# Kernel optimization log

Measured on AMD Instinct MI355X. Metric: run time of the kernel, lower is better.

## Reference

```python
import jax, jax.numpy as jnp
import numpy as np

R = 40            # guided-filter radius (81x81 window)
EPS = 1e-3
BETA = 2.996 / 300.0  # visibility_m = 300.0


def _box_sum(x, r=R):
    """Zero-padded sliding-window sum over an (B,C,H,W) tensor.
    Matches F.avg_pool2d(x, 2r+1, stride=1, padding=r) * (2r+1)^2
    (count_include_pad=True), computed in O(HW) via prefix sums."""
    B, C, H, W = x.shape

    def _along(y, axis, L):
        cs = jnp.cumsum(y, axis=axis)
        pad = [(0, 0)] * 4
        pad[axis] = (1, 0)
        cs = jnp.pad(cs, pad)  # cs[i] = sum of first i elements
        hi = jnp.clip(jnp.arange(L) + r + 1, 0, L)
        lo = jnp.clip(jnp.arange(L) - r, 0, L)
        return jnp.take(cs, hi, axis=axis) - jnp.take(cs, lo, axis=axis)

    x = _along(x, 2, H)
    x = _along(x, 3, W)
    return x


def _guided_filter(I, p, r=R, eps=EPS):
    N = (2 * r + 1) ** 2
    mean_I = _box_sum(I, r) / N
    mean_p = _box_sum(p, r) / N
    mean_Ip = _box_sum(I * p, r) / N
    cov_Ip = mean_Ip - mean_I * mean_p
    mean_II = _box_sum(I * I, r) / N
    var_I = mean_II - mean_I * mean_I
    a = cov_Ip / (var_I + eps)
    b = mean_p - a * mean_I
    mean_a = _box_sum(a, r) / N
    mean_b = _box_sum(b, r) / N
    return mean_a * I + mean_b


def setup_inputs() -> dict:
    key = jax.random.key(0)
    k1, k2 = jax.random.split(key)
    B, H, W = 8, 768, 1280
    img = jax.random.uniform(k1, (B, 3, H, W), dtype=jnp.float32)
    depth = jax.random.uniform(k2, (B, 1, H, W), dtype=jnp.float32) * 500.0
    return {"img": img, "depth": depth}


def reference(img, depth):
    B, _, H, W = img.shape
    t_raw = jnp.clip(jnp.exp(-BETA * depth), 0.0, 1.0)          # (B,1,H,W)
    gray = (0.299 * img[:, 0:1] + 0.587 * img[:, 1:2]
            + 0.114 * img[:, 2:3])                               # (B,1,H,W)
    t = _guided_filter(gray, t_raw)                               # (B,1,H,W)

    # atmospheric light A: mean color over the k farthest pixels, per image
    k = max(10, int(0.001 * H * W))
    k = min(k, H * W)
    depth_flat = depth.reshape(B, -1)                             # (B,HW)
    img_flat = img.reshape(B, 3, -1)                              # (B,3,HW)
    _, idx = jax.lax.top_k(depth_flat, k)                         # (B,k)
    A = jnp.take_along_axis(img_flat, idx[:, None, :], axis=2).mean(axis=2)
    A = A.reshape(B, 3, 1, 1)

    return img * t + A * (1.0 - t)
```

## Files before the change

kernel.cpp:

```cpp
#include <hip/hip_runtime.h>
#include <hip/hip_fp16.h>
#include <stdint.h>

typedef unsigned int u32;

#define Bn 8
#define Hn 768
#define Wn 1280
#define HWs (Hn*Wn)
#define Rr 40
#define NNinv (1.0f/6561.0f)
#define KTOP 983
#define BETA_C (2.996f/300.0f)
#define EQCAP 4096
#define TK_BPI 480
#define NCH 96
#define SEGV 16
#define NSEGV 48
#define HIMG 4
#define TK1_WAVES 16
#define TW 640
#define CW 680

#define OFF_F     0
#define OFF_AB1   (16*HWs)
#define OFF_AB2   (24*HWs)
#define OFF_CS4f  (32*HWs)
#define OFF_CS2f  (36*HWs)
#define OFF_TAILf (38*HWs)

#define OFFH_FOVF 0
#define OFFH_AB   (4*HWs)
#define CS_N      (HIMG*NCH*Wn)
#define OFFH_CS4  (12*HWs)
#define OFFH_CS2  (OFFH_CS4 + 4*CS_N)
#define OFFH_TAIL (OFFH_CS2 + 2*CS_N)

#define ZERO_U32  (Bn*4096 + Bn*65536 + Bn)
#define ZERO_U4   (ZERO_U32/4 + 1)

__device__ __forceinline__ float4 f4add(float4 a, float4 b){ return make_float4(a.x+b.x,a.y+b.y,a.z+b.z,a.w+b.w); }
__device__ __forceinline__ float4 f4sub(float4 a, float4 b){ return make_float4(a.x-b.x,a.y-b.y,a.z-b.z,a.w-b.w); }

__device__ __forceinline__ u32 h2_to_u32(__half2 h){ union { __half2 h; u32 u; } c; c.h = h; return c.u; }
__device__ __forceinline__ __half2 u32_to_h2(u32 u){ union { u32 u; __half2 h; } c; c.u = u; return c.h; }

__global__ __launch_bounds__(256) void fill0_kernel(uint4* __restrict__ p){
  int i = blockIdx.x*256 + threadIdx.x;
  if (i < ZERO_U4) p[i] = make_uint4(0,0,0,0);
}


__global__ __launch_bounds__(256) void gA_kernel(const float* __restrict__ img, const float* __restrict__ depth,
    uint2* __restrict__ F, float4* __restrict__ CS4){
  __shared__ float4 lds[769];
  __shared__ float4 wtot[4];
  int blk = blockIdx.x;
  int xt = blk & 1;
  int t2 = blk >> 1;
  int b = t2 / NCH, ch = t2 % NCH;
  int x0 = xt*TW;
  int cstart = xt ? (TW - Rr) : 0;
  int tid = threadIdx.x;
  int lane = tid & 63, wv = tid >> 6;
  float4 acc[3];
  #pragma unroll
  for (int j = 0; j < 3; ++j) acc[j] = make_float4(0,0,0,0);

  const float* irB = img + ((size_t)(b*3+0)*Hn + ch*8)*Wn + cstart;
  const float* igB = img + ((size_t)(b*3+1)*Hn + ch*8)*Wn + cstart;
  const float* ibB = img + ((size_t)(b*3+2)*Hn + ch*8)*Wn + cstart;
  const float* dpB = depth + ((size_t)b*Hn + ch*8)*Wn + cstart;

  float pr[3], pg[3], pb[3], pd[3];
  #pragma unroll
  for (int j = 0; j < 3; ++j){
    int i = tid + j*256;
    if (i < CW){ pr[j]=irB[i]; pg[j]=igB[i]; pb[j]=ibB[i]; pd[j]=dpB[i]; }
  }

  for (int r = 0; r < 8; ++r){
    int y = ch*8 + r;
    __syncthreads();
    #pragma unroll
    for (int j = 0; j < 3; ++j){
      int i = tid + j*256;
      float4 f = make_float4(0,0,0,0);
      if (i < CW){
        float I = 0.299f*pr[j] + 0.587f*pg[j] + 0.114f*pb[j];
        float p = fminf(fmaxf(expf(-BETA_C*pd[j]), 0.0f), 1.0f);
        f = make_float4(I, p, I*p, I*I);
      }
      lds[i] = f;
    }
    if (r < 7){
      size_t off = (size_t)(r+1)*Wn;
      #pragma unroll
      for (int j = 0; j < 3; ++j){
        int i = tid + j*256;
        if (i < CW){ pr[j]=irB[off+i]; pg[j]=igB[off+i]; pb[j]=ibB[off+i]; pd[j]=dpB[off+i]; }
      }
    }
    __syncthreads();
    int base = tid*3;
    float4 loc[3]; float4 tsum = make_float4(0,0,0,0);
    #pragma unroll
    for (int j = 0; j < 3; ++j){ loc[j] = lds[base+j]; tsum = f4add(tsum, loc[j]); }
    float4 v = tsum;
    for (int d = 1; d < 64; d <<= 1){
      float4 o; o.x = __shfl_up(v.x, d); o.y = __shfl_up(v.y, d); o.z = __shfl_up(v.z, d); o.w = __shfl_up(v.w, d);
      if (lane >= d) v = f4add(v, o);
    }
    if (lane == 63) wtot[wv] = v;
    __syncthreads();
    float4 ex = f4sub(v, tsum);
    for (int w = 0; w < wv; ++w) ex = f4add(ex, wtot[w]);
    float4 run = ex;
    #pragma unroll
    for (int j = 0; j < 3; ++j){ lds[base+j] = run; run = f4add(run, loc[j]); }
    __syncthreads();
    #pragma unroll
    for (int j = 0; j < 3; ++j){
      int lx = tid + j*256;
      if (lx < TW){
        int gx = x0 + lx;
        int hi = gx + Rr + 1; if (hi > Wn) hi = Wn;
        int lo = gx - Rr;     if (lo < 0)  lo = 0;
        float4 s = f4sub(lds[hi - cstart], lds[lo - cstart]);
        __half2 h01 = __float22half2_rn(make_float2(s.x, s.y));
        __half2 h23 = __float22half2_rn(make_float2(s.z, s.w));
        F[(size_t)b*HWs + (size_t)y*Wn + gx] = make_uint2(h2_to_u32(h01), h2_to_u32(h23));
        float2 f0 = __half22float2(h01), f1 = __half22float2(h23);
        acc[j] = f4add(acc[j], make_float4(f0.x, f0.y, f1.x, f1.y));
      }
    }
  }
  #pragma unroll
  for (int j = 0; j < 3; ++j){
    int lx = tid + j*256;
    if (lx < TW) CS4[((size_t)b*NCH + ch)*Wn + x0 + lx] = acc[j];
  }
}

__global__ __launch_bounds__(256) void vAf_kernel(const uint2* __restrict__ F, const float4* __restrict__ CS,
    u32* __restrict__ AB){
  int gt = blockIdx.x*256 + threadIdx.x;
  int x  = gt % Wn;
  int t2 = gt / Wn;
  int b = t2 % Bn, s = t2 / Bn;
  const uint2* Fb   = F + (size_t)b*HWs;
  const float4* CSb = CS + (size_t)b*NCH*Wn;
  int y0 = s*SEGV;
  int c0 = 2*s - 5; if (c0 < 0) c0 = 0;
  int c1 = 2*s + 5; if (c1 > NCH) c1 = NCH;
  float4 S = make_float4(0,0,0,0);
  for (int c = c0; c < c1; ++c) S = f4add(S, CSb[(size_t)c*Wn + x]);
  u32* ABb = AB + (size_t)b*HWs;
  #pragma unroll 8
  for (int y = y0; y < y0 + SEGV; ++y){
    int ya = y + Rr;
    if (ya < Hn){
      uint2 u = Fb[(size_t)ya*Wn + x];
      float2 f0 = __half22float2(u32_to_h2(u.x)), f1 = __half22float2(u32_to_h2(u.y));
      S.x += f0.x; S.y += f0.y; S.z += f1.x; S.w += f1.y;
    }
    float mI = S.x*NNinv, mp = S.y*NNinv, mIp = S.z*NNinv, mII = S.w*NNinv;
    float var = mII - mI*mI;
    float a  = (mIp - mI*mp) / (var + 1e-3f);
    float bb = mp - a*mI;
    ABb[(size_t)y*Wn + x] = h2_to_u32(__float22half2_rn(make_float2(a, bb)));
    int yb = y - Rr;
    if (yb >= 0){
      uint2 u = Fb[(size_t)yb*Wn + x];
      float2 f0 = __half22float2(u32_to_h2(u.x)), f1 = __half22float2(u32_to_h2(u.y));
      S.x -= f0.x; S.y -= f0.y; S.z -= f1.x; S.w -= f1.y;
    }
  }
}

__global__ __launch_bounds__(256) void gB_kernel(const u32* __restrict__ AB1, u32* __restrict__ AB2,
    float2* __restrict__ CS2){
  __shared__ float2 lds[769];
  __shared__ float2 wtot[4];
  int blk = blockIdx.x;
  int xt = blk & 1;
  int t2 = blk >> 1;
  int b = t2 / NCH, ch = t2 % NCH;
  int x0 = xt*TW;
  int cstart = xt ? (TW - Rr) : 0;
  int tid = threadIdx.x;
  int lane = tid & 63, wv = tid >> 6;
  float2 acc[3];
  #pragma unroll
  for (int j = 0; j < 3; ++j) acc[j] = make_float2(0,0);

  const u32* rowB = AB1 + (size_t)b*HWs + (size_t)(ch*8)*Wn + cstart;
  u32 pv[3];
  #pragma unroll
  for (int j = 0; j < 3; ++j){
    int i = tid + j*256;
    if (i < CW) pv[j] = rowB[i];
  }

  for (int r = 0; r < 8; ++r){
    int y = ch*8 + r;
    __syncthreads();
    #pragma unroll
    for (int j = 0; j < 3; ++j){
      int i = tid + j*256;
      float2 f = make_float2(0,0);
      if (i < CW) f = __half22float2(u32_to_h2(pv[j]));
      lds[i] = f;
    }
    if (r < 7){
      size_t off = (size_t)(r+1)*Wn;
      #pragma unroll
      for (int j = 0; j < 3; ++j){
        int i = tid + j*256;
        if (i < CW) pv[j] = rowB[off+i];
      }
    }
    __syncthreads();
    int base = tid*3;
    float2 loc[3]; float2 tsum = make_float2(0,0);
    #pragma unroll
    for (int j = 0; j < 3; ++j){ loc[j] = lds[base+j]; tsum.x += loc[j].x; tsum.y += loc[j].y; }
    float2 v = tsum;
    for (int d = 1; d < 64; d <<= 1){
      float2 o; o.x = __shfl_up(v.x, d); o.y = __shfl_up(v.y, d);
      if (lane >= d){ v.x += o.x; v.y += o.y; }
    }
    if (lane == 63) wtot[wv] = v;
    __syncthreads();
    float2 ex = make_float2(v.x - tsum.x, v.y - tsum.y);
    for (int w = 0; w < wv; ++w){ ex.x += wtot[w].x; ex.y += wtot[w].y; }
    float2 run = ex;
    #pragma unroll
    for (int j = 0; j < 3; ++j){ lds[base+j] = run; run.x += loc[j].x; run.y += loc[j].y; }
    __syncthreads();
    #pragma unroll
    for (int j = 0; j < 3; ++j){
      int lx = tid + j*256;
      if (lx < TW){
        int gx = x0 + lx;
        int hi = gx + Rr + 1; if (hi > Wn) hi = Wn;
        int lo = gx - Rr;     if (lo < 0)  lo = 0;
        float2 s = make_float2(lds[hi - cstart].x - lds[lo - cstart].x,
                               lds[hi - cstart].y - lds[lo - cstart].y);
        __half2 h = __float22half2_rn(s);
        AB2[(size_t)b*HWs + (size_t)y*Wn + gx] = h2_to_u32(h);
        float2 fr = __half22float2(h);
        acc[j].x += fr.x; acc[j].y += fr.y;
      }
    }
  }
  #pragma unroll
  for (int j = 0; j < 3; ++j){
    int lx = tid + j*256;
    if (lx < TW) CS2[((size_t)b*NCH + ch)*Wn + x0 + lx] = acc[j];
  }
}

__global__ __launch_bounds__(256) void vBf_kernel(const u32* __restrict__ AB2, const float2* __restrict__ CS,
    const float* __restrict__ img, const float* __restrict__ Avec, float* __restrict__ out){
  int gt = blockIdx.x*256 + threadIdx.x;
  int x  = gt % Wn;
  int t2 = gt / Wn;
  int b = t2 % Bn, s = t2 / Bn;
  const u32* ABb = AB2 + (size_t)b*HWs;
  const float2* CSb = CS + (size_t)b*NCH*Wn;
  int y0 = s*SEGV;
  int c0 = 2*s - 5; if (c0 < 0) c0 = 0;
  int c1 = 2*s + 5; if (c1 > NCH) c1 = NCH;
  float2 S = make_float2(0,0);
// ... 10 lines not shown
    int ya = y + Rr;
    if (ya < Hn){ float2 t = __half22float2(u32_to_h2(ABb[(size_t)ya*Wn + x])); S.x += t.x; S.y += t.y; }
    float ma = S.x*NNinv, mb = S.y*NNinv;
    size_t idx = (size_t)y*Wn + x;
    float r = ir[idx], g = ig[idx], bb = ib[idx];
    float gray = 0.299f*r + 0.587f*g + 0.114f*bb;
    float t = ma*gray + mb;
    o0[idx] = r *t + A0*(1.0f - t);
    o1[idx] = g *t + A1*(1.0f - t);
    o2[idx] = bb*t + A2*(1.0f - t);
    int yb = y - Rr;
    if (yb >= 0){ float2 t2v = __half22float2(u32_to_h2(ABb[(size_t)yb*Wn + x])); S.x -= t2v.x; S.y -= t2v.y; }
  }
}


__global__ __launch_bounds__(256) void hA_kernel(const float* __restrict__ img, const float* __restrict__ depth,
    float4* __restrict__ Fd, float4* __restrict__ Fw, int half){
  __shared__ float4 lds[Wn+1];
  __shared__ float4 wtot[4];
  int blk = blockIdx.x;
  int bl = blk / Hn, y = blk % Hn;
  int b = half*HIMG + bl;
  const float* ir = img + ((size_t)(b*3+0)*Hn + y)*Wn;
  const float* ig = img + ((size_t)(b*3+1)*Hn + y)*Wn;
  const float* ib = img + ((size_t)(b*3+2)*Hn + y)*Wn;
  const float* dp = depth + ((size_t)b*Hn + y)*Wn;
  int tid = threadIdx.x;
  for (int i = tid; i < Wn; i += 256){
    float r = ir[i], g = ig[i], bb = ib[i];
// ... 142 lines not shown
    if (ya < Hn){ float2 t = ABb[(size_t)ya*Wn + x]; S.x += t.x; S.y += t.y; }
    float ma = S.x*NNinv, mb = S.y*NNinv;
    size_t idx = (size_t)y*Wn + x;
    float r = ir[idx], g = ig[idx], bb = ib[idx];
    float gray = 0.299f*r + 0.587f*g + 0.114f*bb;
    float t = ma*gray + mb;
    o0[idx] = r *t + A0*(1.0f - t);
    o1[idx] = g *t + A1*(1.0f - t);
    o2[idx] = bb*t + A2*(1.0f - t);
    int yb = y - Rr;
    if (yb >= 0){ float2 t2v = ABb[(size_t)yb*Wn + x]; S.x -= t2v.x; S.y -= t2v.y; }
  }
}


__global__ __launch_bounds__(1024) void tk1_kernel(const float* __restrict__ depth, u32* __restrict__ hist1){
  __shared__ u32 lh[TK1_WAVES*2048];
  int tid = threadIdx.x;
  for (int i = tid; i < TK1_WAVES*2048; i += 1024) lh[i] = 0;
  __syncthreads();
  int b = blockIdx.x >> 5;
  int slice = blockIdx.x & 31;
  const int per = HWs/32;
  int start = b*HWs + slice*per;
  u32* h = &lh[(tid >> 6) * 2048];
  const float2* dp = (const float2*)(depth + start);
  for (int i = tid; i < per/2; i += 1024){
    float2 v = dp[i];
    u32 u0 = __float_as_uint(v.x), u1 = __float_as_uint(v.y);
    u32 b0 = u0 >> 20, b1 = u1 >> 20;
    atomicAdd(&h[b0 >> 1], (b0 & 1u) ? 65536u : 1u);
    atomicAdd(&h[b1 >> 1], (b1 & 1u) ? 65536u : 1u);
  }
  __syncthreads();
  for (int i = tid; i < 4096; i += 1024){
    u32 s = 0;
    for (int w = 0; w < TK1_WAVES; ++w) s += (lh[w*2048 + (i>>1)] >> ((i&1)*16)) & 0xFFFFu;
    if (s) atomicAdd(&hist1[b*4096+i], s);
  }
}

__global__ __launch_bounds__(256) void tk2_kernel(const u32* __restrict__ hist1,
    u32* __restrict__ selP1, u32* __restrict__ selK1){
  int b = blockIdx.x, tid = threadIdx.x;
  const u32* h = hist1 + b*4096;
  u32 cs = 0; int bb = tid*16;
  for (int i = 0; i < 16; ++i) cs += h[bb+i];
  __shared__ u32 sums[256];
  sums[tid] = cs; __syncthreads();
  u32 above = 0;
  for (int t = tid+1; t < 256; ++t) above += sums[t];
  if (above < KTOP && above + cs >= KTOP){
    u32 acc = above;
    for (int i = 15; i >= 0; --i){
      u32 c = h[bb+i]; acc += c;
      if (acc >= KTOP){ selP1[b] = (u32)(bb+i); selK1[b] = KTOP - (acc - c); break; }
    }
  }
}

__global__ __launch_bounds__(256) void tk3_kernel(const float* __restrict__ depth,
    const u32* __restrict__ selP1, u32* __restrict__ hist2){
  int idx = blockIdx.x*2048 + threadIdx.x;
  int b = blockIdx.x / TK_BPI;
  u32 p1 = selP1[b];
  for (int it = 0; it < 8; ++it, idx += 256){
    u32 u = __float_as_uint(depth[idx]);
    if ((u>>20) == p1) atomicAdd(&hist2[b*65536 + ((u>>4)&0xFFFFu)], 1u);
  }
}

__global__ __launch_bounds__(256) void tk4_kernel(const u32* __restrict__ hist2, const u32* __restrict__ selP1,
    const u32* __restrict__ selK1, u32* __restrict__ selTau, u32* __restrict__ selK2){
  int b = blockIdx.x, tid = threadIdx.x;
  const u32* h = hist2 + b*65536;
  u32 kk = selK1[b];
  u32 cs = 0; int bb = tid*256;
  for (int i = 0; i < 256; ++i) cs += h[bb+i];
  __shared__ u32 sums[256];
  sums[tid] = cs; __syncthreads();
  u32 above = 0;
  for (int t = tid+1; t < 256; ++t) above += sums[t];
  if (above < kk && above + cs >= kk){
    u32 acc = above;
    for (int i = 255; i >= 0; --i){
      u32 c = h[bb+i]; acc += c;
      if (acc >= kk){ selTau[b] = (selP1[b]<<16) | (u32)(bb+i); selK2[b] = kk - (acc - c); break; }
    }
  }
}

__global__ __launch_bounds__(256) void tk5_kernel(const float* __restrict__ depth, const float* __restrict__ img,
    const u32* __restrict__ selTau, u32* __restrict__ eqCount, u32* __restrict__ eqVal, u32* __restrict__ eqIdx,
    float* __restrict__ partial){
  int blk = blockIdx.x;
  int b = blk / TK_BPI;
  u32 tau = selTau[b];
  int idx = blk*2048 + threadIdx.x;
  float cr = 0.f, cg = 0.f, cb = 0.f;
  for (int it = 0; it < 8; ++it, idx += 256){
    int pix = idx - b*HWs;
    u32 u = __float_as_uint(depth[idx]);
    u32 u28 = u >> 4;
    if (u28 > tau){
      cr += img[(size_t)(b*3+0)*HWs + pix];
      cg += img[(size_t)(b*3+1)*HWs + pix];
      cb += img[(size_t)(b*3+2)*HWs + pix];
    } else if (u28 == tau){
      u32 p = atomicAdd(&eqCount[b], 1u);
      if (p < EQCAP){ eqVal[b*EQCAP+p] = u; eqIdx[b*EQCAP+p] = (u32)pix; }
    }
  }
  for (int d = 32; d; d >>= 1){
    cr += __shfl_down(cr, d); cg += __shfl_down(cg, d); cb += __shfl_down(cb, d);
  }
  __shared__ float wsum[4][3];
  int lane = threadIdx.x & 63, wv = threadIdx.x >> 6;
  if (lane == 0){ wsum[wv][0] = cr; wsum[wv][1] = cg; wsum[wv][2] = cb; }
  __syncthreads();
  if (threadIdx.x == 0){
    float r = 0.f, g = 0.f, bl = 0.f;
    for (int w = 0; w < 4; ++w){ r += wsum[w][0]; g += wsum[w][1]; bl += wsum[w][2]; }
    partial[blk*3+0] = r; partial[blk*3+1] = g; partial[blk*3+2] = bl;
  }
}

__global__ void tk6_kernel(const float* __restrict__ img, const u32* __restrict__ eqCount,
    u32* __restrict__ eqVal, const u32* __restrict__ eqIdx, const u32* __restrict__ selK2,
    const float* __restrict__ partial, float* __restrict__ Avec){
  int b = blockIdx.x;
  int tid = threadIdx.x;
  float r = 0.f, g = 0.f, bl = 0.f;
  for (int i = tid; i < TK_BPI; i += 64){
    r  += partial[(b*TK_BPI+i)*3+0];
    g  += partial[(b*TK_BPI+i)*3+1];
    bl += partial[(b*TK_BPI+i)*3+2];
  }
  for (int d = 32; d; d >>= 1){
    r += __shfl_down(r, d); g += __shfl_down(g, d); bl += __shfl_down(bl, d);
  }
  if (tid != 0) return;
  u32 m = eqCount[b]; if (m > EQCAP) m = EQCAP;
  u32 need = selK2[b]; if (need > m) need = m;
  float cr = r, cg = g, cb = bl;
  for (u32 it = 0; it < need; ++it){
    int best = -1; u32 bv = 0, bi = 0;
    for (u32 j = 0; j < m; ++j){
      u32 vv = eqVal[b*EQCAP+j];
      if (vv == 0xFFFFFFFFu) continue;
      u32 ix = eqIdx[b*EQCAP+j];
      if (best < 0 || vv > bv || (vv == bv && ix < bi)){ best = (int)j; bv = vv; bi = ix; }
    }
    eqVal[b*EQCAP+best] = 0xFFFFFFFFu;
    cr += img[(size_t)(b*3+0)*HWs + bi];
    cg += img[(size_t)(b*3+1)*HWs + bi];
    cb += img[(size_t)(b*3+2)*HWs + bi];
  }
  float inv = 1.0f/(float)KTOP;
  Avec[b*3+0] = cr*inv; Avec[b*3+1] = cg*inv; Avec[b*3+2] = cb*inv;
}


extern "C" void kernel_launch(void* const* d_in, const int* in_sizes, int n_in,
                              void* d_out, int out_size, void* d_ws, size_t ws_size,
                              hipStream_t stream){
  const float* img   = (const float*)d_in[0];
  const float* depth = (const float*)d_in[1];
  float* out = (float*)d_out;
  float* ws  = (float*)d_ws;

  const size_t tailFloats = (size_t)ZERO_U32 + 4*Bn + 2*(size_t)Bn*EQCAP
                          + (size_t)Bn*TK_BPI*3 + Bn*3 + 16;
  const size_t needFull = ((size_t)38*HWs + tailFloats) * sizeof(float);
  bool full = (ws_size >= needFull);

  size_t offTail = full ? (size_t)OFF_TAILf : (size_t)OFFH_TAIL;
  u32* tail    = (u32*)(ws + offTail);
  u32* hist1   = tail;
  u32* hist2   = hist1 + Bn*4096;
  u32* eqCount = hist2 + (size_t)Bn*65536;
  u32* selP1   = eqCount + Bn;
  u32* selK1   = selP1 + Bn;
  u32* selTau  = selK1 + Bn;
  u32* selK2   = selTau + Bn;
  u32* eqVal   = selK2 + Bn;
  u32* eqIdx   = eqVal + (size_t)Bn*EQCAP;
  float* partial = (float*)(eqIdx + (size_t)Bn*EQCAP);
  float* Avec    = partial + (size_t)Bn*TK_BPI*3;

  fill0_kernel<<<dim3((ZERO_U4 + 255)/256), dim3(256), 0, stream>>>((uint4*)tail);

  tk1_kernel<<<dim3(Bn*32), dim3(1024), 0, stream>>>(depth, hist1);
  tk2_kernel<<<dim3(Bn),    dim3(256), 0, stream>>>(hist1, selP1, selK1);
  tk3_kernel<<<dim3(Bn*TK_BPI), dim3(256), 0, stream>>>(depth, selP1, hist2);
  tk4_kernel<<<dim3(Bn),    dim3(256), 0, stream>>>(hist2, selP1, selK1, selTau, selK2);
  tk5_kernel<<<dim3(Bn*TK_BPI), dim3(256), 0, stream>>>(depth, img, selTau, eqCount, eqVal, eqIdx, partial);
  tk6_kernel<<<dim3(Bn),    dim3(64),  0, stream>>>(img, eqCount, eqVal, eqIdx, selK2, partial, Avec);

  if (full){
    uint2*  F   = (uint2*)(ws + OFF_F);
    u32*    AB1 = (u32*)(ws + OFF_AB1);
    u32*    AB2 = (u32*)(ws + OFF_AB2);
    float4* CS4 = (float4*)(ws + OFF_CS4f);
    float2* CS2 = (float2*)(ws + OFF_CS2f);
    gA_kernel <<<dim3(Bn*NCH*2),            dim3(256), 0, stream>>>(img, depth, F, CS4);
    vAf_kernel<<<dim3((Bn*Wn*NSEGV)/256),   dim3(256), 0, stream>>>(F, CS4, AB1);
    gB_kernel <<<dim3(Bn*NCH*2),            dim3(256), 0, stream>>>(AB1, AB2, CS2);
    vBf_kernel<<<dim3((Bn*Wn*NSEGV)/256),   dim3(256), 0, stream>>>(AB2, CS2, img, Avec, out);
  } else {
    float4* Fw  = (float4*)(ws + OFFH_FOVF);
    float2* AB  = (float2*)(ws + OFFH_AB);
    float4* CS4 = (float4*)(ws + OFFH_CS4);
    float2* CS2 = (float2*)(ws + OFFH_CS2);
    for (int half = 0; half < 2; ++half){
      float4* Fd = (float4*)out + (size_t)half*3*HWs;
      hA_kernel <<<dim3(HIMG*Hn),            dim3(256), 0, stream>>>(img, depth, Fd, Fw, half);
      cs4_kernel<<<dim3((HIMG*NCH*Wn)/256),  dim3(256), 0, stream>>>(Fd, Fw, CS4);
      vA_kernel <<<dim3((HIMG*Wn*NSEGV)/256),dim3(256), 0, stream>>>(Fd, Fw, CS4, AB);
      hB_kernel <<<dim3(HIMG*Hn),            dim3(256), 0, stream>>>(AB);
      cs2_kernel<<<dim3((HIMG*NCH*Wn)/256),  dim3(256), 0, stream>>>(AB, CS2);
      vB_kernel <<<dim3((HIMG*Wn*NSEGV)/256),dim3(256), 0, stream>>>(AB, CS2, img, Avec, out, half);
    }
  }
}
// ... 1 lines not shown
```

Before: 220.4 us.

## Fuse top-k histogram passes into guided-filter kernels as extra blocks

Top-k selection stages tk1, tk3 and tk5 are merged into the guided-filter kernels gA, vAf and gB as extra blocks selected by blockIdx. Their independent work can then fill the GPU alongside the filter passes, and the separate launches disappear. The tk1 histogram now uses 256-thread blocks with 4 per-wave histograms instead of 16, and LDS is shared through a union. The fallback path keeps the original separate kernels, and extra LDS per block in gA may reduce occupancy.

```diff
diff --git a/kernel.cpp b/kernel.cpp
--- a/kernel.cpp
+++ b/kernel.cpp
@@ -18,9 +18,10 @@
 #define SEGV 16
 #define NSEGV 48
 #define HIMG 4
-#define TK1_WAVES 16
 #define TW 640
 #define CW 680
+#define NGA (Bn*NCH*2)
+#define NVF ((Bn*Wn*NSEGV)/256)
 
 #define OFF_F     0
 #define OFF_AB1   (16*HWs)
@@ -51,213 +52,282 @@
 }
 
 
-__global__ __launch_bounds__(256) void gA_kernel(const float* __restrict__ img, const float* __restrict__ depth,
-    uint2* __restrict__ F, float4* __restrict__ CS4){
-  __shared__ float4 lds[769];
-  __shared__ float4 wtot[4];
-  int blk = blockIdx.x;
-  int xt = blk & 1;
-  int t2 = blk >> 1;
-  int b = t2 / NCH, ch = t2 % NCH;
-  int x0 = xt*TW;
-  int cstart = xt ? (TW - Rr) : 0;
+__global__ __launch_bounds__(256) void gA_tk1_kernel(const float* __restrict__ img, const float* __restrict__ depth,
+    uint2* __restrict__ F, float4* __restrict__ CS4, u32* __restrict__ hist1){
+  __shared__ union SM {
+    u32 lh[8192];
+    struct { float4 lds[769]; float4 wtot[4]; } g;
+  } sm;
   int tid = threadIdx.x;
-  int lane = tid & 63, wv = tid >> 6;
-  float4 acc[3];
-  #pragma unroll
-  for (int j = 0; j < 3; ++j) acc[j] = make_float4(0,0,0,0);
-
-  const float* irB = img + ((size_t)(b*3+0)*Hn + ch*8)*Wn + cstart;
-  const float* igB = img + ((size_t)(b*3+1)*Hn + ch*8)*Wn + cstart;
-  const float* ibB = img + ((size_t)(b*3+2)*Hn + ch*8)*Wn + cstart;
-  const float* dpB = depth + ((size_t)b*Hn + ch*8)*Wn + cstart;
-
-  float pr[3], pg[3], pb[3], pd[3];
-  #pragma unroll
-  for (int j = 0; j < 3; ++j){
-    int i = tid + j*256;
-    if (i < CW){ pr[j]=irB[i]; pg[j]=igB[i]; pb[j]=ibB[i]; pd[j]=dpB[i]; }
-  }
-
-  for (int r = 0; r < 8; ++r){
-    int y = ch*8 + r;
-    __syncthreads();
+  if ((int)blockIdx.x < NGA){
+    int blk = blockIdx.x;
+    int xt = blk & 1;
+    int t2 = blk >> 1;
+    int b = t2 / NCH, ch = t2 % NCH;
+    int x0 = xt*TW;
+    int cstart = xt ? (TW - Rr) : 0;
+    int lane = tid & 63, wv = tid >> 6;
+    float4 acc[3];
+    #pragma unroll
+    for (int j = 0; j < 3; ++j) acc[j] = make_float4(0,0,0,0);
+    const float* irB = img + ((size_t)(b*3+0)*Hn + ch*8)*Wn + cstart;
+    const float* igB = img + ((size_t)(b*3+1)*Hn + ch*8)*Wn + cstart;
+    const float* ibB = img + ((size_t)(b*3+2)*Hn + ch*8)*Wn + cstart;
+    const float* dpB = depth + ((size_t)b*Hn + ch*8)*Wn + cstart;
+    float pr[3], pg[3], pb[3], pd[3];
     #pragma unroll
     for (int j = 0; j < 3; ++j){
       int i = tid + j*256;
-      float4 f = make_float4(0,0,0,0);
-      if (i < CW){
-        float I = 0.299f*pr[j] + 0.587f*pg[j] + 0.114f*pb[j];
-        float p = fminf(fmaxf(expf(-BETA_C*pd[j]), 0.0f), 1.0f);
-        f = make_float4(I, p, I*p, I*I);
-      }
-      lds[i] = f;
-    }
-    if (r < 7){
-      size_t off = (size_t)(r+1)*Wn;
+      if (i < CW){ pr[j]=irB[i]; pg[j]=igB[i]; pb[j]=ibB[i]; pd[j]=dpB[i]; }
+    }
+    for (int r = 0; r < 8; ++r){
+      int y = ch*8 + r;
+      __syncthreads();
       #pragma unroll
       for (int j = 0; j < 3; ++j){
         int i = tid + j*256;
-        if (i < CW){ pr[j]=irB[off+i]; pg[j]=igB[off+i]; pb[j]=ibB[off+i]; pd[j]=dpB[off+i]; }
-      }
-    }
-    __syncthreads();
-    int base = tid*3;
-    float4 loc[3]; float4 tsum = make_float4(0,0,0,0);
-    #pragma unroll
-    for (int j = 0; j < 3; ++j){ loc[j] = lds[base+j]; tsum = f4add(tsum, loc[j]); }
-    float4 v = tsum;
-    for (int d = 1; d < 64; d <<= 1){
-      float4 o; o.x = __shfl_up(v.x, d); o.y = __shfl_up(v.y, d); o.z = __shfl_up(v.z, d); o.w = __shfl_up(v.w, d);
-      if (lane >= d) v = f4add(v, o);
-    }
-    if (lane == 63) wtot[wv] = v;
-    __syncthreads();
-    float4 ex = f4sub(v, tsum);
-    for (int w = 0; w < wv; ++w) ex = f4add(ex, wtot[w]);
-    float4 run = ex;
-    #pragma unroll
-    for (int j = 0; j < 3; ++j){ lds[base+j] = run; run = f4add(run, loc[j]); }
-    __syncthreads();
+        float4 f = make_float4(0,0,0,0);
+        if (i < CW){
+          float I = 0.299f*pr[j] + 0.587f*pg[j] + 0.114f*pb[j];
+          float p = fminf(fmaxf(expf(-BETA_C*pd[j]), 0.0f), 1.0f);
+          f = make_float4(I, p, I*p, I*I);
+        }
+        sm.g.lds[i] = f;
+      }
+      if (r < 7){
+        size_t off = (size_t)(r+1)*Wn;
+        #pragma unroll
+        for (int j = 0; j < 3; ++j){
+          int i = tid + j*256;
+          if (i < CW){ pr[j]=irB[off+i]; pg[j]=igB[off+i]; pb[j]=ibB[off+i]; pd[j]=dpB[off+i]; }
+        }
+      }
+      __syncthreads();
+      int base = tid*3;
+      float4 loc[3]; float4 tsum = make_float4(0,0,0,0);
+      #pragma unroll
+      for (int j = 0; j < 3; ++j){ loc[j] = sm.g.lds[base+j]; tsum = f4add(tsum, loc[j]); }
+      float4 v = tsum;
+      for (int d = 1; d < 64; d <<= 1){
+        float4 o; o.x = __shfl_up(v.x, d); o.y = __shfl_up(v.y, d); o.z = __shfl_up(v.z, d); o.w = __shfl_up(v.w, d);
+        if (lane >= d) v = f4add(v, o);
+      }
+      if (lane == 63) sm.g.wtot[wv] = v;
+      __syncthreads();
+      float4 ex = f4sub(v, tsum);
+      for (int w = 0; w < wv; ++w) ex = f4add(ex, sm.g.wtot[w]);
+      float4 run = ex;
+      #pragma unroll
+      for (int j = 0; j < 3; ++j){ sm.g.lds[base+j] = run; run = f4add(run, loc[j]); }
+      __syncthreads();
+      #pragma unroll
+      for (int j = 0; j < 3; ++j){
+        int lx = tid + j*256;
+        if (lx < TW){
+          int gx = x0 + lx;
+          int hi = gx + Rr + 1; if (hi > Wn) hi = Wn;
+          int lo = gx - Rr;     if (lo < 0)  lo = 0;
+          float4 s = f4sub(sm.g.lds[hi - cstart], sm.g.lds[lo - cstart]);
+          __half2 h01 = __float22half2_rn(make_float2(s.x, s.y));
+          __half2 h23 = __float22half2_rn(make_float2(s.z, s.w));
+          F[(size_t)b*HWs + (size_t)y*Wn + gx] = make_uint2(h2_to_u32(h01), h2_to_u32(h23));
+          float2 f0 = __half22float2(h01), f1 = __half22float2(h23);
+          acc[j] = f4add(acc[j], make_float4(f0.x, f0.y, f1.x, f1.y));
+        }
+      }
+    }
     #pragma unroll
     for (int j = 0; j < 3; ++j){
       int lx = tid + j*256;
-      if (lx < TW){
-        int gx = x0 + lx;
-        int hi = gx + Rr + 1; if (hi > Wn) hi = Wn;
-        int lo = gx - Rr;     if (lo < 0)  lo = 0;
-        float4 s = f4sub(lds[hi - cstart], lds[lo - cstart]);
-        __half2 h01 = __float22half2_rn(make_float2(s.x, s.y));
-        __half2 h23 = __float22half2_rn(make_float2(s.z, s.w));
-        F[(size_t)b*HWs + (size_t)y*Wn + gx] = make_uint2(h2_to_u32(h01), h2_to_u32(h23));
-        float2 f0 = __half22float2(h01), f1 = __half22float2(h23);
-        acc[j] = f4add(acc[j], make_float4(f0.x, f0.y, f1.x, f1.y));
-      }
-    }
-  }
-  #pragma unroll
-  for (int j = 0; j < 3; ++j){
-    int lx = tid + j*256;
-    if (lx < TW) CS4[((size_t)b*NCH + ch)*Wn + x0 + lx] = acc[j];
-  }
-}
-
-__global__ __launch_bounds__(256) void vAf_kernel(const uint2* __restrict__ F, const float4* __restrict__ CS,
-    u32* __restrict__ AB){
-  int gt = blockIdx.x*256 + threadIdx.x;
-  int x  = gt % Wn;
-  int t2 = gt / Wn;
-  int b = t2 % Bn, s = t2 / Bn;
-  const uint2* Fb   = F + (size_t)b*HWs;
-  const float4* CSb = CS + (size_t)b*NCH*Wn;
-  int y0 = s*SEGV;
-  int c0 = 2*s - 5; if (c0 < 0) c0 = 0;
-  int c1 = 2*s + 5; if (c1 > NCH) c1 = NCH;
-  float4 S = make_float4(0,0,0,0);
-  for (int c = c0; c < c1; ++c) S = f4add(S, CSb[(size_t)c*Wn + x]);
-  u32* ABb = AB + (size_t)b*HWs;
-  #pragma unroll 8
-  for (int y = y0; y < y0 + SEGV; ++y){
-    int ya = y + Rr;
-    if (ya < Hn){
-      uint2 u = Fb[(size_t)ya*Wn + x];
-      float2 f0 = __half22float2(u32_to_h2(u.x)), f1 = __half22float2(u32_to_h2(u.y));
-      S.x += f0.x; S.y += f0.y; S.z += f1.x; S.w += f1.y;
-    }
-    float mI = S.x*NNinv, mp = S.y*NNinv, mIp = S.z*NNinv, mII = S.w*NNinv;
-    float var = mII - mI*mI;
-    float a  = (mIp - mI*mp) / (var + 1e-3f);
-    float bb = mp - a*mI;
-    ABb[(size_t)y*Wn + x] = h2_to_u32(__float22half2_rn(make_float2(a, bb)));
-    int yb = y - Rr;
-    if (yb >= 0){
-      uint2 u = Fb[(size_t)yb*Wn + x];
-      float2 f0 = __half22float2(u32_to_h2(u.x)), f1 = __half22float2(u32_to_h2(u.y));
-      S.x -= f0.x; S.y -= f0.y; S.z -= f1.x; S.w -= f1.y;
-    }
-  }
-}
-
-__global__ __launch_bounds__(256) void gB_kernel(const u32* __restrict__ AB1, u32* __restrict__ AB2,
-    float2* __restrict__ CS2){
-  __shared__ float2 lds[769];
-  __shared__ float2 wtot[4];
-  int blk = blockIdx.x;
-  int xt = blk & 1;
-  int t2 = blk >> 1;
-  int b = t2 / NCH, ch = t2 % NCH;
-  int x0 = xt*TW;
-  int cstart = xt ? (TW - Rr) : 0;
+      if (lx < TW) CS4[((size_t)b*NCH + ch)*Wn + x0 + lx] = acc[j];
+    }
+  } else {
+    for (int i = tid; i < 8192; i += 256) sm.lh[i] = 0;
+    __syncthreads();
+    int blk = blockIdx.x - NGA;
+    int b = blk >> 5;
+    int slice = blk & 31;
+    const int per = HWs/32;
+    int start = b*HWs + slice*per;
+    u32* h = &sm.lh[(tid >> 6) * 2048];
+    const float2* dp = (const float2*)(depth + start);
+    for (int i = tid; i < per/2; i += 256){
+      float2 v = dp[i];
+      u32 u0 = __float_as_uint(v.x), u1 = __float_as_uint(v.y);
+      u32 b0 = u0 >> 20, b1 = u1 >> 20;
+      atomicAdd(&h[b0 >> 1], (b0 & 1u) ? 65536u : 1u);
+      atomicAdd(&h[b1 >> 1], (b1 & 1u) ? 65536u : 1u);
+    }
+    __syncthreads();
+    for (int i = tid; i < 4096; i += 256){
+      u32 s = 0;
+      for (int w = 0; w < 4; ++w) s += (sm.lh[w*2048 + (i>>1)] >> ((i&1)*16)) & 0xFFFFu;
+      if (s) atomicAdd(&hist1[b*4096+i], s);
+    }
+  }
+}
+
+__global__ __launch_bounds__(256) void vAf_tk3_kernel(const uint2* __restrict__ F, const float4* __restrict__ CS,
+    u32* __restrict__ AB, const float* __restrict__ depth, const u32* __restrict__ selP1, u32* __restrict__ hist2){
+  if ((int)blockIdx.x < NVF){
+    int gt = blockIdx.x*256 + threadIdx.x;
+    int x  = gt % Wn;
+    int t2 = gt / Wn;
+    int b = t2 % Bn, s = t2 / Bn;
+    const uint2* Fb   = F + (size_t)b*HWs;
+    const float4* CSb = CS + (size_t)b*NCH*Wn;
+    int y0 = s*SEGV;
+    int c0 = 2*s - 5; if (c0 < 0) c0 = 0;
+    int c1 = 2*s + 5; if (c1 > NCH) c1 = NCH;
+    float4 S = make_float4(0,0,0,0);
+    for (int c = c0; c < c1; ++c) S = f4add(S, CSb[(size_t)c*Wn + x]);
+    u32* ABb = AB + (size_t)b*HWs;
+    #pragma unroll 8
+    for (int y = y0; y < y0 + SEGV; ++y){
+      int ya = y + Rr;
+      if (ya < Hn){
+        uint2 u = Fb[(size_t)ya*Wn + x];
+        float2 f0 = __half22float2(u32_to_h2(u.x)), f1 = __half22float2(u32_to_h2(u.y));
+        S.x += f0.x; S.y += f0.y; S.z += f1.x; S.w += f1.y;
+      }
+      float mI = S.x*NNinv, mp = S.y*NNinv, mIp = S.z*NNinv, mII = S.w*NNinv;
+      float var = mII - mI*mI;
+      float a  = (mIp - mI*mp) / (var + 1e-3f);
+      float bb = mp - a*mI;
+      ABb[(size_t)y*Wn + x] = h2_to_u32(__float22half2_rn(make_float2(a, bb)));
+      int yb = y - Rr;
+      if (yb >= 0){
+        uint2 u = Fb[(size_t)yb*Wn + x];
+        float2 f0 = __half22float2(u32_to_h2(u.x)), f1 = __half22float2(u32_to_h2(u.y));
+        S.x -= f0.x; S.y -= f0.y; S.z -= f1.x; S.w -= f1.y;
+      }
+    }
+  } else {
+    int blk = blockIdx.x - NVF;
+    int idx = blk*2048 + threadIdx.x;
+    int b = blk / TK_BPI;
+    u32 p1 = selP1[b];
+    for (int it = 0; it < 8; ++it, idx += 256){
+      u32 u = __float_as_uint(depth[idx]);
+      if ((u>>20) == p1) atomicAdd(&hist2[b*65536 + ((u>>4)&0xFFFFu)], 1u);
+    }
+  }
+}
+
+__global__ __launch_bounds__(256) void gB_tk5_kernel(const u32* __restrict__ AB1, u32* __restrict__ AB2,
+    float2* __restrict__ CS2, const float* __restrict__ depth, const float* __restrict__ img,
+    const u32* __restrict__ selTau, u32* __restrict__ eqCount, u32* __restrict__ eqVal, u32* __restrict__ eqIdx,
+    float* __restrict__ partial){
+  __shared__ union SM {
+    struct { float2 lds[769]; float2 wtot[4]; } g;
+    float wsum[12];
+  } sm;
   int tid = threadIdx.x;
-  int lane = tid & 63, wv = tid >> 6;
-  float2 acc[3];
-  #pragma unroll
-  for (int j = 0; j < 3; ++j) acc[j] = make_float2(0,0);
-
-  const u32* rowB = AB1 + (size_t)b*HWs + (size_t)(ch*8)*Wn + cstart;
-  u32 pv[3];
-  #pragma unroll
-  for (int j = 0; j < 3; ++j){
-    int i = tid + j*256;
-    if (i < CW) pv[j] = rowB[i];
-  }
-
-  for (int r = 0; r < 8; ++r){
-    int y = ch*8 + r;
-    __syncthreads();
+  if ((int)blockIdx.x < NGA){
+    int blk = blockIdx.x;
+    int xt = blk & 1;
+    int t2 = blk >> 1;
+    int b = t2 / NCH, ch = t2 % NCH;
+    int x0 = xt*TW;
+    int cstart = xt ? (TW - Rr) : 0;
+    int lane = tid & 63, wv = tid >> 6;
+    float2 acc[3];
+    #pragma unroll
+    for (int j = 0; j < 3; ++j) acc[j] = make_float2(0,0);
+    const u32* rowB = AB1 + (size_t)b*HWs + (size_t)(ch*8)*Wn + cstart;
+    u32 pv[3];
     #pragma unroll
     for (int j = 0; j < 3; ++j){
       int i = tid + j*256;
-      float2 f = make_float2(0,0);
-      if (i < CW) f = __half22float2(u32_to_h2(pv[j]));
-      lds[i] = f;
-    }
-    if (r < 7){
-      size_t off = (size_t)(r+1)*Wn;
+      if (i < CW) pv[j] = rowB[i];
+    }
+    for (int r = 0; r < 8; ++r){
+      int y = ch*8 + r;
+      __syncthreads();
       #pragma unroll
       for (int j = 0; j < 3; ++j){
         int i = tid + j*256;
-        if (i < CW) pv[j] = rowB[off+i];
-      }
-    }
-    __syncthreads();
-    int base = tid*3;
-    float2 loc[3]; float2 tsum = make_float2(0,0);
-    #pragma unroll
-    for (int j = 0; j < 3; ++j){ loc[j] = lds[base+j]; tsum.x += loc[j].x; tsum.y += loc[j].y; }
-    float2 v = tsum;
-    for (int d = 1; d < 64; d <<= 1){
-      float2 o; o.x = __shfl_up(v.x, d); o.y = __shfl_up(v.y, d);
-      if (lane >= d){ v.x += o.x; v.y += o.y; }
-    }
-    if (lane == 63) wtot[wv] = v;
-    __syncthreads();
-    float2 ex = make_float2(v.x - tsum.x, v.y - tsum.y);
-    for (int w = 0; w < wv; ++w){ ex.x += wtot[w].x; ex.y += wtot[w].y; }
-    float2 run = ex;
-    #pragma unroll
-    for (int j = 0; j < 3; ++j){ lds[base+j] = run; run.x += loc[j].x; run.y += loc[j].y; }
-    __syncthreads();
+        float2 f = make_float2(0,0);
+        if (i < CW) f = __half22float2(u32_to_h2(pv[j]));
+        sm.g.lds[i] = f;
+      }
+      if (r < 7){
+        size_t off = (size_t)(r+1)*Wn;
+        #pragma unroll
+        for (int j = 0; j < 3; ++j){
+          int i = tid + j*256;
+          if (i < CW) pv[j] = rowB[off+i];
+        }
+      }
+      __syncthreads();
+      int base = tid*3;
+      float2 loc[3]; float2 tsum = make_float2(0,0);
+      #pragma unroll
+      for (int j = 0; j < 3; ++j){ loc[j] = sm.g.lds[base+j]; tsum.x += loc[j].x; tsum.y += loc[j].y; }
+      float2 v = tsum;
+      for (int d = 1; d < 64; d <<= 1){
+        float2 o; o.x = __shfl_up(v.x, d); o.y = __shfl_up(v.y, d);
+        if (lane >= d){ v.x += o.x; v.y += o.y; }
+      }
+      if (lane == 63) sm.g.wtot[wv] = v;
+      __syncthreads();
+      float2 ex = make_float2(v.x - tsum.x, v.y - tsum.y);
+      for (int w = 0; w < wv; ++w){ ex.x += sm.g.wtot[w].x; ex.y += sm.g.wtot[w].y; }
+      float2 run = ex;
+      #pragma unroll
+      for (int j = 0; j < 3; ++j){ sm.g.lds[base+j] = run; run.x += loc[j].x; run.y += loc[j].y; }
+      __syncthreads();
+      #pragma unroll
+      for (int j = 0; j < 3; ++j){
+        int lx = tid + j*256;
+        if (lx < TW){
+          int gx = x0 + lx;
+          int hi = gx + Rr + 1; if (hi > Wn) hi = Wn;
+          int lo = gx - Rr;     if (lo < 0)  lo = 0;
+          float2 s = make_float2(sm.g.lds[hi - cstart].x - sm.g.lds[lo - cstart].x,
+                                 sm.g.lds[hi - cstart].y - sm.g.lds[lo - cstart].y);
+          __half2 h = __float22half2_rn(s);
+          AB2[(size_t)b*HWs + (size_t)y*Wn + gx] = h2_to_u32(h);
+          float2 fr = __half22float2(h);
+          acc[j].x += fr.x; acc[j].y += fr.y;
+        }
+      }
+    }
     #pragma unroll
     for (int j = 0; j < 3; ++j){
       int lx = tid + j*256;
-      if (lx < TW){
-        int gx = x0 + lx;
-        int hi = gx + Rr + 1; if (hi > Wn) hi = Wn;
-        int lo = gx - Rr;     if (lo < 0)  lo = 0;
-        float2 s = make_float2(lds[hi - cstart].x - lds[lo - cstart].x,
-                               lds[hi - cstart].y - lds[lo - cstart].y);
-        __half2 h = __float22half2_rn(s);
-        AB2[(size_t)b*HWs + (size_t)y*Wn + gx] = h2_to_u32(h);
-        float2 fr = __half22float2(h);
-        acc[j].x += fr.x; acc[j].y += fr.y;
-      }
-    }
-  }
-  #pragma unroll
-  for (int j = 0; j < 3; ++j){
-    int lx = tid + j*256;
-    if (lx < TW) CS2[((size_t)b*NCH + ch)*Wn + x0 + lx] = acc[j];
+      if (lx < TW) CS2[((size_t)b*NCH + ch)*Wn + x0 + lx] = acc[j];
+    }
+  } else {
+    int blk = blockIdx.x - NGA;
+    int b = blk / TK_BPI;
+    u32 tau = selTau[b];
+    int idx = blk*2048 + tid;
+    float cr = 0.f, cg = 0.f, cb = 0.f;
+    for (int it = 0; it < 8; ++it, idx += 256){
+      int pix = idx - b*HWs;
+      u32 u = __float_as_uint(depth[idx]);
+      u32 u28 = u >> 4;
+      if (u28 > tau){
+        cr += img[(size_t)(b*3+0)*HWs + pix];
+        cg += img[(size_t)(b*3+1)*HWs + pix];
+        cb += img[(size_t)(b*3+2)*HWs + pix];
+      } else if (u28 == tau){
+        u32 p = atomicAdd(&eqCount[b], 1u);
+        if (p < EQCAP){ eqVal[b*EQCAP+p] = u; eqIdx[b*EQCAP+p] = (u32)pix; }
+      }
+    }
+    for (int d = 32; d; d >>= 1){
+      cr += __shfl_down(cr, d); cg += __shfl_down(cg, d); cb += __shfl_down(cb, d);
+    }
+    int lane = tid & 63, wv = tid >> 6;
+    if (lane == 0){ sm.wsum[wv*3+0] = cr; sm.wsum[wv*3+1] = cg; sm.wsum[wv*3+2] = cb; }
+    __syncthreads();
+    if (tid == 0){
+      float r = 0.f, g = 0.f, bl = 0.f;
+      for (int w = 0; w < 4; ++w){ r += sm.wsum[w*3+0]; g += sm.wsum[w*3+1]; bl += sm.wsum[w*3+2]; }
+      partial[blk*3+0] = r; partial[blk*3+1] = g; partial[blk*3+2] = bl;
+    }
   }
 }
 
@@ -298,6 +368,153 @@
   }
 }
 
+
+__global__ __launch_bounds__(256) void tk2_kernel(const u32* __restrict__ hist1,
+    u32* __restrict__ selP1, u32* __restrict__ selK1){
+  int b = blockIdx.x, tid = threadIdx.x;
+  const u32* h = hist1 + b*4096;
+  u32 cs = 0; int bb = tid*16;
+  for (int i = 0; i < 16; ++i) cs += h[bb+i];
+  __shared__ u32 sums[256];
+  sums[tid] = cs; __syncthreads();
+  u32 above = 0;
+  for (int t = tid+1; t < 256; ++t) above += sums[t];
+  if (above < KTOP && above + cs >= KTOP){
+    u32 acc = above;
+    for (int i = 15; i >= 0; --i){
+      u32 c = h[bb+i]; acc += c;
+      if (acc >= KTOP){ selP1[b] = (u32)(bb+i); selK1[b] = KTOP - (acc - c); break; }
+    }
+  }
+}
+
+__global__ __launch_bounds__(256) void tk4_kernel(const u32* __restrict__ hist2, const u32* __restrict__ selP1,
+    const u32* __restrict__ selK1, u32* __restrict__ selTau, u32* __restrict__ selK2){
+  int b = blockIdx.x, tid = threadIdx.x;
+  const u32* h = hist2 + b*65536;
+  u32 kk = selK1[b];
+  u32 cs = 0; int bb = tid*256;
+  for (int i = 0; i < 256; ++i) cs += h[bb+i];
+  __shared__ u32 sums[256];
+  sums[tid] = cs; __syncthreads();
+  u32 above = 0;
+  for (int t = tid+1; t < 256; ++t) above += sums[t];
+  if (above < kk && above + cs >= kk){
+    u32 acc = above;
+    for (int i = 255; i >= 0; --i){
+      u32 c = h[bb+i]; acc += c;
+      if (acc >= kk){ selTau[b] = (selP1[b]<<16) | (u32)(bb+i); selK2[b] = kk - (acc - c); break; }
+    }
+  }
+}
+
+__global__ void tk6_kernel(const float* __restrict__ img, const u32* __restrict__ eqCount,
+    u32* __restrict__ eqVal, const u32* __restrict__ eqIdx, const u32* __restrict__ selK2,
+    const float* __restrict__ partial, float* __restrict__ Avec){
+  int b = blockIdx.x;
+  int tid = threadIdx.x;
+  float r = 0.f, g = 0.f, bl = 0.f;
+  for (int i = tid; i < TK_BPI; i += 64){
+    r  += partial[(b*TK_BPI+i)*3+0];
+    g  += partial[(b*TK_BPI+i)*3+1];
+    bl += partial[(b*TK_BPI+i)*3+2];
+  }
+  for (int d = 32; d; d >>= 1){
+    r += __shfl_down(r, d); g += __shfl_down(g, d); bl += __shfl_down(bl, d);
+  }
+  if (tid != 0) return;
+  u32 m = eqCount[b]; if (m > EQCAP) m = EQCAP;
+  u32 need = selK2[b]; if (need > m) need = m;
+  float cr = r, cg = g, cb = bl;
+  for (u32 it = 0; it < need; ++it){
+    int best = -1; u32 bv = 0, bi = 0;
+    for (u32 j = 0; j < m; ++j){
+      u32 vv = eqVal[b*EQCAP+j];
+      if (vv == 0xFFFFFFFFu) continue;
+      u32 ix = eqIdx[b*EQCAP+j];
+      if (best < 0 || vv > bv || (vv == bv && ix < bi)){ best = (int)j; bv = vv; bi = ix; }
+    }
+    eqVal[b*EQCAP+best] = 0xFFFFFFFFu;
+    cr += img[(size_t)(b*3+0)*HWs + bi];
+    cg += img[(size_t)(b*3+1)*HWs + bi];
+    cb += img[(size_t)(b*3+2)*HWs + bi];
+  }
+  float inv = 1.0f/(float)KTOP;
+  Avec[b*3+0] = cr*inv; Avec[b*3+1] = cg*inv; Avec[b*3+2] = cb*inv;
+}
+
+
+__global__ __launch_bounds__(1024) void tk1_kernel(const float* __restrict__ depth, u32* __restrict__ hist1){
+  __shared__ u32 lh[16*2048];
+  int tid = threadIdx.x;
+  for (int i = tid; i < 16*2048; i += 1024) lh[i] = 0;
+  __syncthreads();
+  int b = blockIdx.x >> 5;
+  int slice = blockIdx.x & 31;
+  const int per = HWs/32;
+  int start = b*HWs + slice*per;
+  u32* h = &lh[(tid >> 6) * 2048];
+  const float2* dp = (const float2*)(depth + start);
+  for (int i = tid; i < per/2; i += 1024){
+    float2 v = dp[i];
+    u32 u0 = __float_as_uint(v.x), u1 = __float_as_uint(v.y);
+    u32 b0 = u0 >> 20, b1 = u1 >> 20;
+    atomicAdd(&h[b0 >> 1], (b0 & 1u) ? 65536u : 1u);
+    atomicAdd(&h[b1 >> 1], (b1 & 1u) ? 65536u : 1u);
+  }
+  __syncthreads();
+  for (int i = tid; i < 4096; i += 1024){
+    u32 s = 0;
+    for (int w = 0; w < 16; ++w) s += (lh[w*2048 + (i>>1)] >> ((i&1)*16)) & 0xFFFFu;
+    if (s) atomicAdd(&hist1[b*4096+i], s);
+  }
+}
+
+__global__ __launch_bounds__(256) void tk3_kernel(const float* __restrict__ depth,
+    const u32* __restrict__ selP1, u32* __restrict__ hist2){
+  int idx = blockIdx.x*2048 + threadIdx.x;
+  int b = blockIdx.x / TK_BPI;
+  u32 p1 = selP1[b];
+  for (int it = 0; it < 8; ++it, idx += 256){
+    u32 u = __float_as_uint(depth[idx]);
+    if ((u>>20) == p1) atomicAdd(&hist2[b*65536 + ((u>>4)&0xFFFFu)], 1u);
+  }
+}
+
+__global__ __launch_bounds__(256) void tk5_kernel(const float* __restrict__ depth, const float* __restrict__ img,
+    const u32* __restrict__ selTau, u32* __restrict__ eqCount, u32* __restrict__ eqVal, u32* __restrict__ eqIdx,
+    float* __restrict__ partial){
+  int blk = blockIdx.x;
+  int b = blk / TK_BPI;
+  u32 tau = selTau[b];
+  int idx = blk*2048 + threadIdx.x;
+  float cr = 0.f, cg = 0.f, cb = 0.f;
+  for (int it = 0; it < 8; ++it, idx += 256){
+    int pix = idx - b*HWs;
+    u32 u = __float_as_uint(depth[idx]);
+    u32 u28 = u >> 4;
+    if (u28 > tau){
+      cr += img[(size_t)(b*3+0)*HWs + pix];
+      cg += img[(size_t)(b*3+1)*HWs + pix];
+      cb += img[(size_t)(b*3+2)*HWs + pix];
+    } else if (u28 == tau){
+      u32 p = atomicAdd(&eqCount[b], 1u);
+      if (p < EQCAP){ eqVal[b*EQCAP+p] = u; eqIdx[b*EQCAP+p] = (u32)pix; }
+    }
+  }
+  for (int d = 32; d; d >>= 1){
+    cr += __shfl_down(cr, d); cg += __shfl_down(cg, d); cb += __shfl_down(cb, d);
+  }
+  __shared__ float wsum[4][3];
+  int lane = threadIdx.x & 63, wv = threadIdx.x >> 6;
+  if (lane == 0){ wsum[wv][0] = cr; wsum[wv][1] = cg; wsum[wv][2] = cb; }
+  __syncthreads();
+  if (threadIdx.x == 0){
+    float r = 0.f, g = 0.f, bl = 0.f;
+    for (int w = 0; w < 4; ++w){ r += wsum[w][0]; g += wsum[w][1]; bl += wsum[w][2]; }
+    partial[blk*3+0] = r; partial[blk*3+1] = g; partial[blk*3+2] = bl;
+  }
+}
 
 __global__ __launch_bounds__(256) void hA_kernel(const float* __restrict__ img, const float* __restrict__ depth,
     float4* __restrict__ Fd, float4* __restrict__ Fw, int half){
@@ -470,153 +687,6 @@
 }
 
 
-__global__ __launch_bounds__(1024) void tk1_kernel(const float* __restrict__ depth, u32* __restrict__ hist1){
-  __shared__ u32 lh[TK1_WAVES*2048];
-  int tid = threadIdx.x;
-  for (int i = tid; i < TK1_WAVES*2048; i += 1024) lh[i] = 0;
-  __syncthreads();
-  int b = blockIdx.x >> 5;
-  int slice = blockIdx.x & 31;
-  const int per = HWs/32;
-  int start = b*HWs + slice*per;
-  u32* h = &lh[(tid >> 6) * 2048];
-  const float2* dp = (const float2*)(depth + start);
-  for (int i = tid; i < per/2; i += 1024){
-    float2 v = dp[i];
-    u32 u0 = __float_as_uint(v.x), u1 = __float_as_uint(v.y);
-    u32 b0 = u0 >> 20, b1 = u1 >> 20;
-    atomicAdd(&h[b0 >> 1], (b0 & 1u) ? 65536u : 1u);
-    atomicAdd(&h[b1 >> 1], (b1 & 1u) ? 65536u : 1u);
-  }
-  __syncthreads();
-  for (int i = tid; i < 4096; i += 1024){
-    u32 s = 0;
-    for (int w = 0; w < TK1_WAVES; ++w) s += (lh[w*2048 + (i>>1)] >> ((i&1)*16)) & 0xFFFFu;
-    if (s) atomicAdd(&hist1[b*4096+i], s);
-  }
-}
-
-__global__ __launch_bounds__(256) void tk2_kernel(const u32* __restrict__ hist1,
-    u32* __restrict__ selP1, u32* __restrict__ selK1){
-  int b = blockIdx.x, tid = threadIdx.x;
-  const u32* h = hist1 + b*4096;
-  u32 cs = 0; int bb = tid*16;
-  for (int i = 0; i < 16; ++i) cs += h[bb+i];
-  __shared__ u32 sums[256];
-  sums[tid] = cs; __syncthreads();
-  u32 above = 0;
-  for (int t = tid+1; t < 256; ++t) above += sums[t];
-  if (above < KTOP && above + cs >= KTOP){
-    u32 acc = above;
-    for (int i = 15; i >= 0; --i){
-      u32 c = h[bb+i]; acc += c;
-      if (acc >= KTOP){ selP1[b] = (u32)(bb+i); selK1[b] = KTOP - (acc - c); break; }
-    }
-  }
-}
-
-__global__ __launch_bounds__(256) void tk3_kernel(const float* __restrict__ depth,
-    const u32* __restrict__ selP1, u32* __restrict__ hist2){
-  int idx = blockIdx.x*2048 + threadIdx.x;
-  int b = blockIdx.x / TK_BPI;
-  u32 p1 = selP1[b];
-  for (int it = 0; it < 8; ++it, idx += 256){
-    u32 u = __float_as_uint(depth[idx]);
-    if ((u>>20) == p1) atomicAdd(&hist2[b*65536 + ((u>>4)&0xFFFFu)], 1u);
-  }
-}
-
-__global__ __launch_bounds__(256) void tk4_kernel(const u32* __restrict__ hist2, const u32* __restrict__ selP1,
-    const u32* __restrict__ selK1, u32* __restrict__ selTau, u32* __restrict__ selK2){
-  int b = blockIdx.x, tid = threadIdx.x;
-  const u32* h = hist2 + b*65536;
-  u32 kk = selK1[b];
-  u32 cs = 0; int bb = tid*256;
-  for (int i = 0; i < 256; ++i) cs += h[bb+i];
-  __shared__ u32 sums[256];
-  sums[tid] = cs; __syncthreads();
-  u32 above = 0;
-  for (int t = tid+1; t < 256; ++t) above += sums[t];
-  if (above < kk && above + cs >= kk){
-    u32 acc = above;
-    for (int i = 255; i >= 0; --i){
-      u32 c = h[bb+i]; acc += c;
-      if (acc >= kk){ selTau[b] = (selP1[b]<<16) | (u32)(bb+i); selK2[b] = kk - (acc - c); break; }
-    }
-  }
-}
-
-__global__ __launch_bounds__(256) void tk5_kernel(const float* __restrict__ depth, const float* __restrict__ img,
-    const u32* __restrict__ selTau, u32* __restrict__ eqCount, u32* __restrict__ eqVal, u32* __restrict__ eqIdx,
-    float* __restrict__ partial){
-  int blk = blockIdx.x;
-  int b = blk / TK_BPI;
-  u32 tau = selTau[b];
-  int idx = blk*2048 + threadIdx.x;
-  float cr = 0.f, cg = 0.f, cb = 0.f;
-  for (int it = 0; it < 8; ++it, idx += 256){
-    int pix = idx - b*HWs;
-    u32 u = __float_as_uint(depth[idx]);
-    u32 u28 = u >> 4;
-    if (u28 > tau){
-      cr += img[(size_t)(b*3+0)*HWs + pix];
-      cg += img[(size_t)(b*3+1)*HWs + pix];
-      cb += img[(size_t)(b*3+2)*HWs + pix];
-    } else if (u28 == tau){
-      u32 p = atomicAdd(&eqCount[b], 1u);
-      if (p < EQCAP){ eqVal[b*EQCAP+p] = u; eqIdx[b*EQCAP+p] = (u32)pix; }
-    }
-  }
-  for (int d = 32; d; d >>= 1){
-    cr += __shfl_down(cr, d); cg += __shfl_down(cg, d); cb += __shfl_down(cb, d);
-  }
-  __shared__ float wsum[4][3];
-  int lane = threadIdx.x & 63, wv = threadIdx.x >> 6;
-  if (lane == 0){ wsum[wv][0] = cr; wsum[wv][1] = cg; wsum[wv][2] = cb; }
-  __syncthreads();
-  if (threadIdx.x == 0){
-    float r = 0.f, g = 0.f, bl = 0.f;
-    for (int w = 0; w < 4; ++w){ r += wsum[w][0]; g += wsum[w][1]; bl += wsum[w][2]; }
-    partial[blk*3+0] = r; partial[blk*3+1] = g; partial[blk*3+2] = bl;
-  }
-}
-
-__global__ void tk6_kernel(const float* __restrict__ img, const u32* __restrict__ eqCount,
-    u32* __restrict__ eqVal, const u32* __restrict__ eqIdx, const u32* __restrict__ selK2,
-    const float* __restrict__ partial, float* __restrict__ Avec){
-  int b = blockIdx.x;
-  int tid = threadIdx.x;
-  float r = 0.f, g = 0.f, bl = 0.f;
-  for (int i = tid; i < TK_BPI; i += 64){
-    r  += partial[(b*TK_BPI+i)*3+0];
-    g  += partial[(b*TK_BPI+i)*3+1];
-    bl += partial[(b*TK_BPI+i)*3+2];
-  }
-  for (int d = 32; d; d >>= 1){
-    r += __shfl_down(r, d); g += __shfl_down(g, d); bl += __shfl_down(bl, d);
-  }
-  if (tid != 0) return;
-  u32 m = eqCount[b]; if (m > EQCAP) m = EQCAP;
-  u32 need = selK2[b]; if (need > m) need = m;
-  float cr = r, cg = g, cb = bl;
-  for (u32 it = 0; it < need; ++it){
-    int best = -1; u32 bv = 0, bi = 0;
-    for (u32 j = 0; j < m; ++j){
-      u32 vv = eqVal[b*EQCAP+j];
-      if (vv == 0xFFFFFFFFu) continue;
-      u32 ix = eqIdx[b*EQCAP+j];
-      if (best < 0 || vv > bv || (vv == bv && ix < bi)){ best = (int)j; bv = vv; bi = ix; }
-    }
-    eqVal[b*EQCAP+best] = 0xFFFFFFFFu;
-    cr += img[(size_t)(b*3+0)*HWs + bi];
-    cg += img[(size_t)(b*3+1)*HWs + bi];
-    cb += img[(size_t)(b*3+2)*HWs + bi];
-  }
-  float inv = 1.0f/(float)KTOP;
-  Avec[b*3+0] = cr*inv; Avec[b*3+1] = cg*inv; Avec[b*3+2] = cb*inv;
-}
-
-
 extern "C" void kernel_launch(void* const* d_in, const int* in_sizes, int n_in,
                               void* d_out, int out_size, void* d_ws, size_t ws_size,
                               hipStream_t stream){
@@ -646,24 +716,27 @@
 
   fill0_kernel<<<dim3((ZERO_U4 + 255)/256), dim3(256), 0, stream>>>((uint4*)tail);
 
-  tk1_kernel<<<dim3(Bn*32), dim3(1024), 0, stream>>>(depth, hist1);
-  tk2_kernel<<<dim3(Bn),    dim3(256), 0, stream>>>(hist1, selP1, selK1);
-  tk3_kernel<<<dim3(Bn*TK_BPI), dim3(256), 0, stream>>>(depth, selP1, hist2);
-  tk4_kernel<<<dim3(Bn),    dim3(256), 0, stream>>>(hist2, selP1, selK1, selTau, selK2);
-  tk5_kernel<<<dim3(Bn*TK_BPI), dim3(256), 0, stream>>>(depth, img, selTau, eqCount, eqVal, eqIdx, partial);
-  tk6_kernel<<<dim3(Bn),    dim3(64),  0, stream>>>(img, eqCount, eqVal, eqIdx, selK2, partial, Avec);
-
   if (full){
     uint2*  F   = (uint2*)(ws + OFF_F);
     u32*    AB1 = (u32*)(ws + OFF_AB1);
     u32*    AB2 = (u32*)(ws + OFF_AB2);
     float4* CS4 = (float4*)(ws + OFF_CS4f);
     float2* CS2 = (float2*)(ws + OFF_CS2f);
-    gA_kernel <<<dim3(Bn*NCH*2),            dim3(256), 0, stream>>>(img, depth, F, CS4);
-    vAf_kernel<<<dim3((Bn*Wn*NSEGV)/256),   dim3(256), 0, stream>>>(F, CS4, AB1);
-    gB_kernel <<<dim3(Bn*NCH*2),            dim3(256), 0, stream>>>(AB1, AB2, CS2);
-    vBf_kernel<<<dim3((Bn*Wn*NSEGV)/256),   dim3(256), 0, stream>>>(AB2, CS2, img, Avec, out);
+    gA_tk1_kernel<<<dim3(NGA + Bn*32),      dim3(256), 0, stream>>>(img, depth, F, CS4, hist1);
+    tk2_kernel   <<<dim3(Bn),               dim3(256), 0, stream>>>(hist1, selP1, selK1);
+    vAf_tk3_kernel<<<dim3(NVF + Bn*TK_BPI), dim3(256), 0, stream>>>(F, CS4, AB1, depth, selP1, hist2);
+    tk4_kernel   <<<dim3(Bn),               dim3(256), 0, stream>>>(hist2, selP1, selK1, selTau, selK2);
+    gB_tk5_kernel<<<dim3(NGA + Bn*TK_BPI),  dim3(256), 0, stream>>>(AB1, AB2, CS2, depth, img, selTau,
+                                                                    eqCount, eqVal, eqIdx, partial);
+    tk6_kernel   <<<dim3(Bn),               dim3(64),  0, stream>>>(img, eqCount, eqVal, eqIdx, selK2, partial, Avec);
+    vBf_kernel   <<<dim3(NVF),              dim3(256), 0, stream>>>(AB2, CS2, img, Avec, out);
   } else {
+    tk1_kernel<<<dim3(Bn*32), dim3(1024), 0, stream>>>(depth, hist1);
+    tk2_kernel<<<dim3(Bn),    dim3(256), 0, stream>>>(hist1, selP1, selK1);
+    tk3_kernel<<<dim3(Bn*TK_BPI), dim3(256), 0, stream>>>(depth, selP1, hist2);
+    tk4_kernel<<<dim3(Bn),    dim3(256), 0, stream>>>(hist2, selP1, selK1, selTau, selK2);
+    tk5_kernel<<<dim3(Bn*TK_BPI), dim3(256), 0, stream>>>(depth, img, selTau, eqCount, eqVal, eqIdx, partial);
+    tk6_kernel<<<dim3(Bn),    dim3(64),  0, stream>>>(img, eqCount, eqVal, eqIdx, selK2, partial, Avec);
     float4* Fw  = (float4*)(ws + OFFH_FOVF);
     float2* AB  = (float2*)(ws + OFFH_AB);
     float4* CS4 = (float4*)(ws + OFFH_CS4);
```

After: 212.7 us. 3.5% less time.
